# Optimization experiments

Measured on AMD Instinct MI355X. Metric: run time of the kernel, lower is better.

Reference implementation:

```python
import jax, jax.numpy as jnp
import numpy as np

T, H, I, E, K = 2048, 1024, 768, 32, 4  # tokens, hidden, expert intermediate, n_experts, top_k


def setup_inputs() -> dict:
    key = jax.random.key(0)
    k0, k1, k2, k3, k4 = jax.random.split(key, 5)
    scale = 0.02
    return {
        "x": jax.random.normal(k0, (T, H), dtype=jnp.float32),
        "gate_w": jax.random.normal(k1, (E, H), dtype=jnp.float32) * scale,   # router linear [E, H]
        "w_gate": jax.random.normal(k2, (E, I, H), dtype=jnp.float32) * scale,  # gate_proj per expert
        "w_up": jax.random.normal(k3, (E, I, H), dtype=jnp.float32) * scale,    # up_proj per expert
        "w_down": jax.random.normal(k4, (E, H, I), dtype=jnp.float32) * scale,  # down_proj per expert
    }


def reference(x, gate_w, w_gate, w_up, w_down):
    # Router: dense gate linear + softmax + top-k + renormalize
    logits = x @ gate_w.T                              # [T, E]
    probs = jax.nn.softmax(logits, axis=-1)
    top_w, top_i = jax.lax.top_k(probs, K)             # [T, K]
    top_w = top_w / jnp.sum(top_w, axis=-1, keepdims=True)  # renormalize=True
    # Dense combine weights [T, E] (zero for unselected experts)
    tok = jnp.arange(T, dtype=jnp.int32)[:, None]
    combine = jnp.zeros((T, E), dtype=x.dtype).at[tok, top_i].add(top_w)

    # Scan over experts: each expert is a SwiGLU MLP; masked-dense combine.
    def step(acc, ws):
        w1, w3, w2, ce = ws                            # [I,H], [I,H], [H,I], [T]
        h = (jax.nn.silu(x @ w1.T) * (x @ w3.T)) @ w2.T  # [T, H]
        return acc + ce[:, None] * h, None

    out, _ = jax.lax.scan(step, jnp.zeros_like(x), (w_gate, w_up, w_down, combine.T))
    return out
```

## Files before the change

### kernel.cpp

```cpp
#include <hip/hip_runtime.h>
#include <hip/hip_bf16.h>
#include <stdint.h>

#define T_TOK 2048
#define HDIM  1024
#define IDIM  768
#define NEXP  32
#define TOPK  4
#define NPAIR (T_TOK*TOPK)
#define MTILE 256
#define MAXMT 64

typedef __attribute__((ext_vector_type(8))) short bf16x8;
typedef __attribute__((ext_vector_type(4))) float f32x4;

typedef __attribute__((address_space(1))) const unsigned int gu32;
typedef __attribute__((address_space(3))) unsigned int lu32;

__device__ __forceinline__ void gload_lds16(const void* g, void* l){
  __builtin_amdgcn_global_load_lds((gu32*)g, (lu32*)l, 16, 0, 0);
}

__device__ __forceinline__ unsigned short f2bf(float f){
  union { float f; unsigned u; } v; v.f = f;
  unsigned r = (v.u + 0x7fffu + ((v.u >> 16) & 1u)) >> 16;
  return (unsigned short)r;
}

__global__ __launch_bounds__(256) void k_convert_x(const float* __restrict__ x,
                                                   ushort* __restrict__ xb){
  int idx = blockIdx.x*256 + threadIdx.x;
  float4 v = ((const float4*)x)[idx];
  ushort4 o; o.x=f2bf(v.x); o.y=f2bf(v.y); o.z=f2bf(v.z); o.w=f2bf(v.w);
  ((ushort4*)xb)[idx] = o;
}

__global__ __launch_bounds__(256) void k_router(const float* __restrict__ x,
                                                const float* __restrict__ gw,
                                                int* __restrict__ ei, float* __restrict__ wv,
                                                int* __restrict__ counts){
  int wid  = threadIdx.x >> 6;
  int lane = threadIdx.x & 63;
  int t = blockIdx.x*4 + wid;
  float xv[16];
  #pragma unroll
  for (int i=0;i<16;i++) xv[i] = x[t*HDIM + i*64 + lane];
  float p[NEXP];
  #pragma unroll
  for (int e=0;e<NEXP;e++){
    const float* w = gw + e*HDIM;
    float a = 0.f;
    #pragma unroll
    for (int i=0;i<16;i++) a = fmaf(xv[i], w[i*64+lane], a);
    #pragma unroll
    for (int off=32; off>=1; off>>=1) a += __shfl_xor(a, off, 64);
    p[e] = a;
  }
  float m = p[0];
  #pragma unroll
  for (int e=1;e<NEXP;e++) m = fmaxf(m, p[e]);
  #pragma unroll
  for (int e=0;e<NEXP;e++) p[e] = __expf(p[e]-m);
  unsigned used = 0; int sel[TOPK]; float sw[TOPK]; float wsum = 0.f;
  #pragma unroll
  for (int k=0;k<TOPK;k++){
    float best = -1.f; int bi = 0;
    #pragma unroll
    for (int e=0;e<NEXP;e++){
      bool ok = (((used>>e)&1u)==0u) && (p[e] > best);
      best = ok ? p[e] : best; bi = ok ? e : bi;
    }
    used |= 1u<<bi; sel[k]=bi; sw[k]=best; wsum += best;
  }
  if (lane==0){
    float inv = 1.f/wsum;
    #pragma unroll
    for (int k=0;k<TOPK;k++){
      ei[t*TOPK+k] = sel[k];
      wv[t*TOPK+k] = sw[k]*inv;
      atomicAdd(&counts[sel[k]], 1);
    }
  }
}

__global__ void k_offsets(const int* __restrict__ counts, int* __restrict__ offsets,
                          int* __restrict__ mtE, int* __restrict__ mtM0,
                          int* __restrict__ nmt){
  if (threadIdx.x==0 && blockIdx.x==0){
    int s=0;
    for (int e=0;e<NEXP;e++){ offsets[e]=s; s+=counts[e]; }
    offsets[NEXP]=s;
    int nm=0;
    for (int e=0;e<NEXP;e++){
      int ne = counts[e];
      for (int m0=0; m0<ne && nm<MAXMT; m0+=MTILE){ mtE[nm]=e; mtM0[nm]=m0; nm++; }
    }
    nmt[0]=nm;
  }
}

__global__ __launch_bounds__(256) void k_scatter(const int* __restrict__ ei,
                                                 const int* __restrict__ offsets,
                                                 int* __restrict__ cursor,
                                                 int* __restrict__ slot_tk,
                                                 int* __restrict__ tk_slot){
  int g = blockIdx.x*256 + threadIdx.x;
  int e = ei[g];
  int pos = atomicAdd(&cursor[e], 1);
  int slot = offsets[e] + pos;
  slot_tk[slot] = g;
  tk_slot[g] = slot;
}

__global__ __launch_bounds__(512,4) void k_gateup(const ushort* __restrict__ xb,
    const float* __restrict__ w1, const float* __restrict__ w3,
    const int* __restrict__ offsets, const int* __restrict__ slot_tk,
    const int* __restrict__ mtE, const int* __restrict__ mtM0, const int* __restrict__ nmt,
    ushort* __restrict__ act){
  int bi  = blockIdx.x;
  int mti = bi / 24;
  int it  = bi - mti*24;
  if (mti >= nmt[0]) return;
  int e    = mtE[mti];
  int m0   = mtM0[mti];
  int off0 = offsets[e];
  int ne   = offsets[e+1]-off0;
  int ibase = it*32;

  __shared__ ushort Als[2][256][32];
  __shared__ float  Bls[2][2][32][32];
  __shared__ int toks[256];

  int tid = threadIdx.x, wid = tid>>6, lane = tid&63;
  if (tid < 256){
    int slot = off0 + m0 + tid;
    int fb = slot_tk[off0] >> 2;
    toks[tid] = (m0 + tid < ne) ? (slot_tk[slot] >> 2) : fb;
  }
  __syncthreads();

  const ushort* asrc0 = xb + (size_t)toks[      wid*16 + (lane>>2)]*HDIM + (lane&3)*8;
  const ushort* asrc1 = xb + (size_t)toks[128 + wid*16 + (lane>>2)]*HDIM + (lane&3)*8;
  int brow = wid*8 + (lane>>3);
  int bmat = brow>>5, birow = brow&31, bc = lane&7;
  const float* bsrc = (bmat ? w3 : w1) + (size_t)e*IDIM*HDIM
                    + (size_t)(ibase+birow)*HDIM + ((bc ^ (birow&7))<<2);

  int wm = wid>>1, wn = wid&1;
  f32x4 accg[4], accu[4];
  #pragma unroll
  for (int m=0;m<4;m++){ accg[m]=(f32x4){0,0,0,0}; accu[m]=(f32x4){0,0,0,0}; }

  ushort* aDst0 = &Als[0][0][0] + (size_t)(      wid*16)*32;
  ushort* aDst1 = &Als[0][0][0] + (size_t)(128 + wid*16)*32;
  float*  bDst  = &Bls[0][0][0][0] + (size_t)wid*256;
  const size_t aBufStride = 256*32;
  const size_t bBufStride = 2*32*32;

  auto stage = [&](int buf, int kb){
    gload_lds16(asrc0 + kb*32, aDst0 + buf*aBufStride);
    gload_lds16(asrc1 + kb*32, aDst1 + buf*aBufStride);
    gload_lds16(bsrc  + kb*32, bDst  + buf*bBufStride);
  };
  int rB = wn*16 + (lane&15);
  int q  = lane>>4;
  int c1 = ( 2*q   ) ^ (rB&7);
  int c2 = ( 2*q+1 ) ^ (rB&7);
  auto compute = [&](int buf){
    bf16x8 af[4];
    #pragma unroll
    for (int m=0;m<4;m++)
      af[m] = *(const bf16x8*)(&Als[buf][wm*64 + m*16 + (lane&15)][q*8]);
    #pragma unroll
    for (int mat=0; mat<2; ++mat){
      f32x4 x1 = *(const f32x4*)(&Bls[buf][mat][rB][c1*4]);
      f32x4 x2 = *(const f32x4*)(&Bls[buf][mat][rB][c2*4]);
      bf16x8 b;
      b[0]=(short)f2bf(x1[0]); b[1]=(short)f2bf(x1[1]);
      b[2]=(short)f2bf(x1[2]); b[3]=(short)f2bf(x1[3]);
      b[4]=(short)f2bf(x2[0]); b[5]=(short)f2bf(x2[1]);
      b[6]=(short)f2bf(x2[2]); b[7]=(short)f2bf(x2[3]);
      if (mat==0){
        #pragma unroll
        for (int m=0;m<4;m++) accg[m] = __builtin_amdgcn_mfma_f32_16x16x32_bf16(af[m], b, accg[m], 0,0,0);
      } else {
        #pragma unroll
        for (int m=0;m<4;m++) accu[m] = __builtin_amdgcn_mfma_f32_16x16x32_bf16(af[m], b, accu[m], 0,0,0);
      }
    }
  };

  stage(0, 0);
  __syncthreads();
  for (int kb=0; kb<32; ++kb){
    int cur = kb & 1;
    if (kb+1 < 32) stage(cur^1, kb+1);
    compute(cur);
    __syncthreads();
  }

  int nval = ne - m0; if (nval > 256) nval = 256;
  #pragma unroll
  for (int m=0;m<4;m++)
    #pragma unroll
    for (int r=0;r<4;r++){
      int row = wm*64 + m*16 + (lane>>4)*4 + r;
      if (row < nval){
        float g = accg[m][r], u = accu[m][r];
        float sval = g / (1.f + __expf(-g)) * u;
        act[(size_t)(off0+m0+row)*IDIM + ibase + wn*16 + (lane&15)] = f2bf(sval);
      }
    }
}

__global__ __launch_bounds__(512,4) void k_down(const ushort* __restrict__ act,
    const float* __restrict__ w2, const int* __restrict__ offsets,
    const int* __restrict__ mtE, const int* __restrict__ mtM0, const int* __restrict__ nmt,
    float* __restrict__ pout){
  int bi  = blockIdx.x;
  int mti = bi >> 4;
  int ht  = bi & 15;
  if (mti >= nmt[0]) return;
  int e    = mtE[mti];
  int m0   = mtM0[mti];
  int off0 = offsets[e], ne = offsets[e+1]-off0;
  int hbase = ht*64;

  __shared__ ushort Als[2][256][32];
  __shared__ float  Bls[2][64][32];

  int tid = threadIdx.x, wid = tid>>6, lane = tid&63;

  int ar0 = m0 +       wid*16 + (lane>>2); ar0 = (ar0 < ne) ? ar0 : (ne-1);
  int ar1 = m0 + 128 + wid*16 + (lane>>2); ar1 = (ar1 < ne) ? ar1 : (ne-1);
  const ushort* asrc0 = act + (size_t)(off0+ar0)*IDIM + (lane&3)*8;
  const ushort* asrc1 = act + (size_t)(off0+ar1)*IDIM + (lane&3)*8;
  int brow = wid*8 + (lane>>3);
  int bc   = lane&7;
  const float* bsrc = w2 + (size_t)e*HDIM*IDIM
                    + (size_t)(hbase+brow)*IDIM + ((bc ^ (brow&7))<<2);

  int wm = wid>>1, wn = wid&1;
  f32x4 acc[4][2];
  #pragma unroll
  for (int m=0;m<4;m++)
    #pragma unroll
    for (int n=0;n<2;n++) acc[m][n]=(f32x4){0,0,0,0};

  ushort* aDst0 = &Als[0][0][0] + (size_t)(      wid*16)*32;
  ushort* aDst1 = &Als[0][0][0] + (size_t)(128 + wid*16)*32;
  float*  bDst  = &Bls[0][0][0] + (size_t)wid*256;
  const size_t aBufStride = 256*32;
  const size_t bBufStride = 64*32;

  auto stage = [&](int buf, int kb){
    gload_lds16(asrc0 + kb*32, aDst0 + buf*aBufStride);
    gload_lds16(asrc1 + kb*32, aDst1 + buf*aBufStride);
    gload_lds16(bsrc  + kb*32, bDst  + buf*bBufStride);
  };
  int q = lane>>4;
  auto compute = [&](int buf){
    bf16x8 af[4];
    #pragma unroll
    for (int m=0;m<4;m++)
      af[m] = *(const bf16x8*)(&Als[buf][wm*64 + m*16 + (lane&15)][q*8]);
    #pragma unroll
    for (int n=0;n<2;n++){
      int rB = wn*32 + n*16 + (lane&15);
      int c1 = ( 2*q   ) ^ (rB&7);
      int c2 = ( 2*q+1 ) ^ (rB&7);
      f32x4 x1 = *(const f32x4*)(&Bls[buf][rB][c1*4]);
      f32x4 x2 = *(const f32x4*)(&Bls[buf][rB][c2*4]);
      bf16x8 b;
      b[0]=(short)f2bf(x1[0]); b[1]=(short)f2bf(x1[1]);
      b[2]=(short)f2bf(x1[2]); b[3]=(short)f2bf(x1[3]);
      b[4]=(short)f2bf(x2[0]); b[5]=(short)f2bf(x2[1]);
      b[6]=(short)f2bf(x2[2]); b[7]=(short)f2bf(x2[3]);
      #pragma unroll
      for (int m=0;m<4;m++)
        acc[m][n] = __builtin_amdgcn_mfma_f32_16x16x32_bf16(af[m], b, acc[m][n], 0,0,0);
    }
  };

  stage(0, 0);
  __syncthreads();
  for (int kb=0; kb<24; ++kb){
    int cur = kb & 1;
    if (kb+1 < 24) stage(cur^1, kb+1);
    compute(cur);
    __syncthreads();
  }

  int nval = ne - m0; if (nval > 256) nval = 256;
  #pragma unroll
  for (int m=0;m<4;m++)
    #pragma unroll
    for (int n=0;n<2;n++)
      #pragma unroll
      for (int r=0;r<4;r++){
        int row = wm*64 + m*16 + (lane>>4)*4 + r;
        if (row < nval)
          pout[(size_t)(off0+m0+row)*HDIM + hbase + wn*32 + n*16 + (lane&15)] = acc[m][n][r];
      }
}

__global__ __launch_bounds__(256) void k_combine(const float* __restrict__ pout,
    const int* __restrict__ tk_slot, const float* __restrict__ wv,
    float* __restrict__ out){
  int t = blockIdx.x;
  int c = threadIdx.x;
  float a0=0,a1=0,a2=0,a3=0;
  #pragma unroll
  for (int k=0;k<TOPK;k++){
    int slot = tk_slot[t*TOPK+k];
    float w  = wv[t*TOPK+k];
    float4 v = *(const float4*)(pout + (size_t)slot*HDIM + c*4);
    a0 = fmaf(w, v.x, a0); a1 = fmaf(w, v.y, a1);
    a2 = fmaf(w, v.z, a2); a3 = fmaf(w, v.w, a3);
  }
  float4 o; o.x=a0; o.y=a1; o.z=a2; o.w=a3;
  *(float4*)(out + (size_t)t*HDIM + c*4) = o;
}

extern "C" void kernel_launch(void* const* d_in, const int* in_sizes, int n_in,
                              void* d_out, int out_size, void* d_ws, size_t ws_size,
                              hipStream_t stream){
  const float* x  = (const float*)d_in[0];
  const float* gw = (const float*)d_in[1];
  const float* w1 = (const float*)d_in[2];
  const float* w3 = (const float*)d_in[3];
  const float* w2 = (const float*)d_in[4];
  float* out = (float*)d_out;

  char* ws = (char*)d_ws;
  size_t off = 0;
  ushort* xb   = (ushort*)(ws + off); off += (size_t)T_TOK*HDIM*2;
  ushort* act  = (ushort*)(ws + off); off += (size_t)NPAIR*IDIM*2;
  float*  pout = (float*) (ws + off); off += (size_t)NPAIR*HDIM*4;
  int* counts  = (int*)(ws + off); off += NEXP*4;
  int* cursor  = (int*)(ws + off); off += NEXP*4;
  int* offsets = (int*)(ws + off); off += (NEXP+1)*4;
  int* mtE     = (int*)(ws + off); off += MAXMT*4;
  int* mtM0    = (int*)(ws + off); off += MAXMT*4;
  int* nmt     = (int*)(ws + off); off += 4;
  off = (off + 255) & ~(size_t)255;
  int*   ei      = (int*)  (ws + off); off += (size_t)NPAIR*4;
  float* wvp     = (float*)(ws + off); off += (size_t)NPAIR*4;
  int*   slot_tk = (int*)  (ws + off); off += (size_t)NPAIR*4;
  int*   tk_slot = (int*)  (ws + off); off += (size_t)NPAIR*4;

  hipMemsetAsync(counts, 0, 2*NEXP*4, stream);

  k_convert_x<<<T_TOK*HDIM/1024, 256, 0, stream>>>(x, xb);
  k_router<<<T_TOK/4, 256, 0, stream>>>(x, gw, ei, wvp, counts);
  k_offsets<<<1, 64, 0, stream>>>(counts, offsets, mtE, mtM0, nmt);
  k_scatter<<<NPAIR/256, 256, 0, stream>>>(ei, offsets, cursor, slot_tk, tk_slot);
  k_gateup<<<MAXMT*24, 512, 0, stream>>>(xb, w1, w3, offsets, slot_tk, mtE, mtM0, nmt, act);
  k_down<<<MAXMT*16, 512, 0, stream>>>(act, w2, offsets, mtE, mtM0, nmt, pout);
  k_combine<<<T_TOK, 256, 0, stream>>>(pout, tk_slot, wvp, out);
}
```

Measured before the change: 270.6 us.

## Triple-buffer MoE GEMM pipelines with explicit vmcnt waits, LDS swizzle, and block reorder

Both expert GEMM kernels move from double to triple buffering, keeping two global-to-LDS loads in flight and waiting on explicit vmcnt counts plus raw barriers instead of __syncthreads. The A-tile LDS layout gets an XOR swizzle to reduce bank conflicts on fragment reads. The fp32-to-bf16 conversion now uses packed hardware conversion, and the block index mapping is reordered to group 8 M-tiles per column tile for better weight reuse in L2. The extra buffer raises LDS use per block, which may reduce occupancy.

Result: slower. 288.7 us (median of 2 runs) (+6.7%).

```diff
diff --git a/kernel.cpp b/kernel.cpp
--- a/kernel.cpp
+++ b/kernel.cpp
@@ -21,10 +21,19 @@
   __builtin_amdgcn_global_load_lds((gu32*)g, (lu32*)l, 16, 0, 0);
 }
 
+#define WAITV(n) asm volatile("s_waitcnt vmcnt(" #n ")" ::: "memory")
+#define BAR()    __builtin_amdgcn_s_barrier()
+
 __device__ __forceinline__ unsigned short f2bf(float f){
   union { float f; unsigned u; } v; v.f = f;
   unsigned r = (v.u + 0x7fffu + ((v.u >> 16) & 1u)) >> 16;
   return (unsigned short)r;
+}
+
+__device__ __forceinline__ unsigned pack_bf2(float lo, float hi){
+  __hip_bfloat162 h2 = __float22bfloat162_rn(float2{lo, hi});
+  union { __hip_bfloat162 h; unsigned u; } v; v.h = h2;
+  return v.u;
 }
 
 __global__ __launch_bounds__(256) void k_convert_x(const float* __restrict__ x,
@@ -118,8 +127,9 @@
     const int* __restrict__ mtE, const int* __restrict__ mtM0, const int* __restrict__ nmt,
     ushort* __restrict__ act){
   int bi  = blockIdx.x;
-  int mti = bi / 24;
-  int it  = bi - mti*24;
+  int s   = bi >> 3;
+  int mti = (s/24)*8 + (bi&7);
+  int it  = s % 24;
   if (mti >= nmt[0]) return;
   int e    = mtE[mti];
   int m0   = mtM0[mti];
@@ -127,9 +137,11 @@
   int ne   = offsets[e+1]-off0;
   int ibase = it*32;
 
-  __shared__ ushort Als[2][256][32];
-  __shared__ float  Bls[2][2][32][32];
+  __shared__ ushort Als[3][256][32];
+  __shared__ float  Bls[3][2][32][32];
   __shared__ int toks[256];
+  const int ABUF = 256*32;
+  const int BBUF = 2*32*32;
 
   int tid = threadIdx.x, wid = tid>>6, lane = tid&63;
   if (tid < 256){
@@ -139,47 +151,51 @@
   }
   __syncthreads();
 
-  const ushort* asrc0 = xb + (size_t)toks[      wid*16 + (lane>>2)]*HDIM + (lane&3)*8;
-  const ushort* asrc1 = xb + (size_t)toks[128 + wid*16 + (lane>>2)]*HDIM + (lane&3)*8;
+  int aswz = (lane&3) ^ ((lane>>3)&3);
+  const ushort* asrc0 = xb + (size_t)toks[      wid*16 + (lane>>2)]*HDIM + aswz*8;
+  const ushort* asrc1 = xb + (size_t)toks[128 + wid*16 + (lane>>2)]*HDIM + aswz*8;
   int brow = wid*8 + (lane>>3);
-  int bmat = brow>>5, birow = brow&31, bc = lane&7;
+  int bmat = brow>>5, birow = brow&31;
   const float* bsrc = (bmat ? w3 : w1) + (size_t)e*IDIM*HDIM
-                    + (size_t)(ibase+birow)*HDIM + ((bc ^ (birow&7))<<2);
+                    + (size_t)(ibase+birow)*HDIM + (((lane&7) ^ (birow&7))<<2);
+
+  ushort* aB = &Als[0][0][0];
+  float*  bB = &Bls[0][0][0][0];
+  ushort* aDst0 = aB + (      wid*16)*32;
+  ushort* aDst1 = aB + (128 + wid*16)*32;
+  float*  bDst  = bB + wid*256;
 
   int wm = wid>>1, wn = wid&1;
   f32x4 accg[4], accu[4];
   #pragma unroll
   for (int m=0;m<4;m++){ accg[m]=(f32x4){0,0,0,0}; accu[m]=(f32x4){0,0,0,0}; }
 
-  ushort* aDst0 = &Als[0][0][0] + (size_t)(      wid*16)*32;
-  ushort* aDst1 = &Als[0][0][0] + (size_t)(128 + wid*16)*32;
-  float*  bDst  = &Bls[0][0][0][0] + (size_t)wid*256;
-  const size_t aBufStride = 256*32;
-  const size_t bBufStride = 2*32*32;
-
   auto stage = [&](int buf, int kb){
-    gload_lds16(asrc0 + kb*32, aDst0 + buf*aBufStride);
-    gload_lds16(asrc1 + kb*32, aDst1 + buf*aBufStride);
-    gload_lds16(bsrc  + kb*32, bDst  + buf*bBufStride);
+    gload_lds16(asrc0 + kb*32, aDst0 + buf*ABUF);
+    gload_lds16(asrc1 + kb*32, aDst1 + buf*ABUF);
+    gload_lds16(bsrc  + kb*32, bDst  + buf*BBUF);
   };
+
+  int q  = lane>>4;
+  int pA = q ^ (((lane&15)>>1)&3);
   int rB = wn*16 + (lane&15);
-  int q  = lane>>4;
-  int c1 = ( 2*q   ) ^ (rB&7);
-  int c2 = ( 2*q+1 ) ^ (rB&7);
+  int c1 = (2*q) ^ (rB&7);
+  int c2 = c1 ^ 1;
   auto compute = [&](int buf){
+    const ushort* Ab = aB + buf*ABUF;
+    const float*  Bb = bB + buf*BBUF;
     bf16x8 af[4];
     #pragma unroll
     for (int m=0;m<4;m++)
-      af[m] = *(const bf16x8*)(&Als[buf][wm*64 + m*16 + (lane&15)][q*8]);
+      af[m] = *(const bf16x8*)(Ab + (wm*64 + m*16 + (lane&15))*32 + pA*8);
     #pragma unroll
     for (int mat=0; mat<2; ++mat){
-      f32x4 x1 = *(const f32x4*)(&Bls[buf][mat][rB][c1*4]);
-      f32x4 x2 = *(const f32x4*)(&Bls[buf][mat][rB][c2*4]);
-      bf16x8 b;
-      b[0]=(short)f2bf(x1[0]); b[1]=(short)f2bf(x1[1]);
-      b[2]=(short)f2bf(x1[2]); b[3]=(short)f2bf(x1[3]);
-      b[4]=(short)f2bf(x2[0]); b[5]=(short)f2bf(x2[1]);
-      b[6]=(short)f2bf(x2[2]); b[7]=(short)f2bf(x2[3]);
+      const float* Br = Bb + (mat*32 + rB)*32;
+      f32x4 x1 = *(const f32x4*)(Br + c1*4);
+      f32x4 x2 = *(const f32x4*)(Br + c2*4);
+      uint4 uu; uu.x=pack_bf2(x1[0],x1[1]); uu.y=pack_bf2(x1[2],x1[3]);
+      uu.z=pack_bf2(x2[0],x2[1]); uu.w=pack_bf2(x2[2],x2[3]);
+      bf16x8 b = *reinterpret_cast<bf16x8*>(&uu);
       if (mat==0){
         #pragma unroll
         for (int m=0;m<4;m++) accg[m] = __builtin_amdgcn_mfma_f32_16x16x32_bf16(af[m], b, accg[m], 0,0,0);
@@ -190,13 +206,15 @@
     }
   };
 
-  stage(0, 0);
-  __syncthreads();
+  stage(0,0);
+  stage(1,1);
   for (int kb=0; kb<32; ++kb){
-    int cur = kb & 1;
-    if (kb+1 < 32) stage(cur^1, kb+1);
-    compute(cur);
-    __syncthreads();
+    if (kb < 30){ stage((kb+2)%3, kb+2); WAITV(6); }
+    else if (kb == 30){ WAITV(3); }
+    else { WAITV(0); }
+    BAR();
+    compute(kb%3);
+    BAR();
   }
 
   int nval = ne - m0; if (nval > 256) nval = 256;
@@ -218,27 +236,36 @@
     const int* __restrict__ mtE, const int* __restrict__ mtM0, const int* __restrict__ nmt,
     float* __restrict__ pout){
   int bi  = blockIdx.x;
-  int mti = bi >> 4;
-  int ht  = bi & 15;
+  int s   = bi >> 3;
+  int mti = (s>>4)*8 + (bi&7);
+  int ht  = s & 15;
   if (mti >= nmt[0]) return;
   int e    = mtE[mti];
   int m0   = mtM0[mti];
   int off0 = offsets[e], ne = offsets[e+1]-off0;
   int hbase = ht*64;
 
-  __shared__ ushort Als[2][256][32];
-  __shared__ float  Bls[2][64][32];
+  __shared__ ushort Als[3][256][32];
+  __shared__ float  Bls[3][64][32];
+  const int ABUF = 256*32;
+  const int BBUF = 64*32;
 
   int tid = threadIdx.x, wid = tid>>6, lane = tid&63;
 
+  int aswz = (lane&3) ^ ((lane>>3)&3);
   int ar0 = m0 +       wid*16 + (lane>>2); ar0 = (ar0 < ne) ? ar0 : (ne-1);
   int ar1 = m0 + 128 + wid*16 + (lane>>2); ar1 = (ar1 < ne) ? ar1 : (ne-1);
-  const ushort* asrc0 = act + (size_t)(off0+ar0)*IDIM + (lane&3)*8;
-  const ushort* asrc1 = act + (size_t)(off0+ar1)*IDIM + (lane&3)*8;
+  const ushort* asrc0 = act + (size_t)(off0+ar0)*IDIM + aswz*8;
+  const ushort* asrc1 = act + (size_t)(off0+ar1)*IDIM + aswz*8;
   int brow = wid*8 + (lane>>3);
-  int bc   = lane&7;
   const float* bsrc = w2 + (size_t)e*HDIM*IDIM
-                    + (size_t)(hbase+brow)*IDIM + ((bc ^ (brow&7))<<2);
+                    + (size_t)(hbase+brow)*IDIM + (((lane&7) ^ (brow&7))<<2);
+
+  ushort* aB = &Als[0][0][0];
+  float*  bB = &Bls[0][0][0];
+  ushort* aDst0 = aB + (      wid*16)*32;
+  ushort* aDst1 = aB + (128 + wid*16)*32;
+  float*  bDst  = bB + wid*256;
 
   int wm = wid>>1, wn = wid&1;
   f32x4 acc[4][2];
@@ -247,48 +274,46 @@
     #pragma unroll
     for (int n=0;n<2;n++) acc[m][n]=(f32x4){0,0,0,0};
 
-  ushort* aDst0 = &Als[0][0][0] + (size_t)(      wid*16)*32;
-  ushort* aDst1 = &Als[0][0][0] + (size_t)(128 + wid*16)*32;
-  float*  bDst  = &Bls[0][0][0] + (size_t)wid*256;
-  const size_t aBufStride = 256*32;
-  const size_t bBufStride = 64*32;
-
   auto stage = [&](int buf, int kb){
-    gload_lds16(asrc0 + kb*32, aDst0 + buf*aBufStride);
-    gload_lds16(asrc1 + kb*32, aDst1 + buf*aBufStride);
-    gload_lds16(bsrc  + kb*32, bDst  + buf*bBufStride);
+    gload_lds16(asrc0 + kb*32, aDst0 + buf*ABUF);
+    gload_lds16(asrc1 + kb*32, aDst1 + buf*ABUF);
+    gload_lds16(bsrc  + kb*32, bDst  + buf*BBUF);
   };
-  int q = lane>>4;
+
+  int q  = lane>>4;
+  int pA = q ^ (((lane&15)>>1)&3);
   auto compute = [&](int buf){
+    const ushort* Ab = aB + buf*ABUF;
+    const float*  Bb = bB + buf*BBUF;
     bf16x8 af[4];
     #pragma unroll
     for (int m=0;m<4;m++)
-      af[m] = *(const bf16x8*)(&Als[buf][wm*64 + m*16 + (lane&15)][q*8]);
+      af[m] = *(const bf16x8*)(Ab + (wm*64 + m*16 + (lane&15))*32 + pA*8);
     #pragma unroll
     for (int n=0;n<2;n++){
       int rB = wn*32 + n*16 + (lane&15);
-      int c1 = ( 2*q   ) ^ (rB&7);
-      int c2 = ( 2*q+1 ) ^ (rB&7);
-      f32x4 x1 = *(const f32x4*)(&Bls[buf][rB][c1*4]);
-      f32x4 x2 = *(const f32x4*)(&Bls[buf][rB][c2*4]);
-      bf16x8 b;
-      b[0]=(short)f2bf(x1[0]); b[1]=(short)f2bf(x1[1]);
-      b[2]=(short)f2bf(x1[2]); b[3]=(short)f2bf(x1[3]);
-      b[4]=(short)f2bf(x2[0]); b[5]=(short)f2bf(x2[1]);
-      b[6]=(short)f2bf(x2[2]); b[7]=(short)f2bf(x2[3]);
+      int c1 = (2*q) ^ (rB&7);
+      const float* Br = Bb + rB*32;
+      f32x4 x1 = *(const f32x4*)(Br + c1*4);
+      f32x4 x2 = *(const f32x4*)(Br + (c1^1)*4);
+      uint4 uu; uu.x=pack_bf2(x1[0],x1[1]); uu.y=pack_bf2(x1[2],x1[3]);
+      uu.z=pack_bf2(x2[0],x2[1]); uu.w=pack_bf2(x2[2],x2[3]);
+      bf16x8 b = *reinterpret_cast<bf16x8*>(&uu);
       #pragma unroll
       for (int m=0;m<4;m++)
         acc[m][n] = __builtin_amdgcn_mfma_f32_16x16x32_bf16(af[m], b, acc[m][n], 0,0,0);
     }
   };
 
-  stage(0, 0);
-  __syncthreads();
+  stage(0,0);
+  stage(1,1);
   for (int kb=0; kb<24; ++kb){
-    int cur = kb & 1;
-    if (kb+1 < 24) stage(cur^1, kb+1);
-    compute(cur);
-    __syncthreads();
+    if (kb < 22){ stage((kb+2)%3, kb+2); WAITV(6); }
+    else if (kb == 22){ WAITV(3); }
+    else { WAITV(0); }
+    BAR();
+    compute(kb%3);
+    BAR();
   }
 
   int nval = ne - m0; if (nval > 256) nval = 256;
```
